# Optimization experiments

Hardware: AMD Instinct MI355X
Metric: run time of the kernel (lower is better)

## Reference

```python
import jax, jax.numpy as jnp
import numpy as np

NUM_CODONS = 64  # len(CODON_MAP_DNA)


def setup_inputs() -> dict:
    key = jax.random.key(0)
    k1, k2, k3, k4 = jax.random.split(key, 4)
    B, S = 16384, 2048
    rna_data = jax.random.randint(k1, (B, S), 0, 65, dtype=jnp.int64 if jax.config.read('jax_enable_x64') else jnp.int32)
    tissue_id = jax.random.randint(k2, (B,), 0, 30, dtype=jnp.int32)
    W = jax.random.normal(k3, (1, NUM_CODONS), dtype=jnp.float32)
    b = jax.random.normal(k4, (1,), dtype=jnp.float32)
    return {"rna_data": rna_data, "tissue_id": tissue_id, "W": W, "b": b}


def _frequencies(rna_data):
    # Batched histogram: counts[b, v] = #{s : rna_data[b, s] == v}, v in [0, 65)
    B = rna_data.shape[0]
    counts = jnp.zeros((B, NUM_CODONS + 1), dtype=jnp.float32)
    counts = counts.at[jnp.arange(B)[:, None], rna_data].add(1.0)
    counts = counts[:, 1:NUM_CODONS + 1]  # drop padding bin 0 -> [B, 64]
    return counts / jnp.sum(counts, axis=1, keepdims=True)


def reference(rna_data, tissue_id, W, b):
    freqs = _frequencies(rna_data)          # [B, 64]
    y_pred = freqs @ W.T + b                # [B, 1]
    return y_pred
```

## Files before the change

kernel.cpp:

```cpp
#include <hip/hip_runtime.h>


__global__ __launch_bounds__(256) void codon_freq_dot_kernel(
    const int* __restrict__ rna,
    const float* __restrict__ W,
    const float* __restrict__ b,
    float* __restrict__ out,
    int S)
{
    __shared__ float Wl[64];
    __shared__ float psum[4];
    __shared__ int   pcnt[4];

    const int row = blockIdx.x;
    const int t   = threadIdx.x;

    if (t < 64) Wl[t] = W[t];
    __syncthreads();

    const int4* p = reinterpret_cast<const int4*>(rna + (size_t)row * (size_t)S);
    const int nvec = S >> 2;

    float sum = 0.0f;
    int   cnt = 0;

    for (int i = t; i < nvec; i += 256) {
        int4 v = p[i];
        int e;
        e = v.x; if (e > 0) { sum += Wl[e - 1]; ++cnt; }
        e = v.y; if (e > 0) { sum += Wl[e - 1]; ++cnt; }
        e = v.z; if (e > 0) { sum += Wl[e - 1]; ++cnt; }
        e = v.w; if (e > 0) { sum += Wl[e - 1]; ++cnt; }
    }

    #pragma unroll
    for (int off = 32; off > 0; off >>= 1) {
        sum += __shfl_down(sum, off, 64);
        cnt += __shfl_down(cnt, off, 64);
    }

    const int wave = t >> 6;
    const int lane = t & 63;
    if (lane == 0) { psum[wave] = sum; pcnt[wave] = cnt; }
    __syncthreads();

    if (t == 0) {
        float s = psum[0] + psum[1] + psum[2] + psum[3];
        int   c = pcnt[0] + pcnt[1] + pcnt[2] + pcnt[3];
        out[row] = s / (float)c + b[0];
    }
}

extern "C" void kernel_launch(void* const* d_in, const int* in_sizes, int n_in,
                              void* d_out, int out_size, void* d_ws, size_t ws_size,
                              hipStream_t stream) {
    const int*   rna = (const int*)d_in[0];
    const float* W   = (const float*)d_in[2];
    const float* b   = (const float*)d_in[3];
    float*       out = (float*)d_out;

    const int B = out_size;
    const int S = in_sizes[0] / B;

    codon_freq_dot_kernel<<<B, 256, 0, stream>>>(rna, W, b, out, S);
}
```

Before: 25.97 us.

## Map one wavefront per row with fully unrolled nontemporal vector loads

Adds a specialized kernel for S=2048 where each wavefront handles a whole row, so a 256-thread block covers four rows. Each lane issues eight 16-byte nontemporal loads up front, and the row is reduced with wave shuffles only, with no shared-memory partials or second barrier. This is meant to raise memory-level parallelism, cut per-row block overhead and avoid polluting the cache on a streaming read. The generic kernel gains a scalar fallback for S not divisible by 4, and the fast path applies only when S is 2048 and B is a multiple of 4.

```diff
diff --git a/kernel.cpp b/kernel.cpp
--- a/kernel.cpp
+++ b/kernel.cpp
@@ -1,5 +1,52 @@
 #include <hip/hip_runtime.h>
 
+
+typedef int int4v __attribute__((ext_vector_type(4)));
+
+template<int NV>
+__global__ __launch_bounds__(256) void codon_rows_kernel(
+    const int* __restrict__ rna,
+    const float* __restrict__ W,
+    const float* __restrict__ b,
+    float* __restrict__ out,
+    int S)
+{
+    __shared__ float Wl[64];
+    const int t = threadIdx.x;
+    if (t < 64) Wl[t] = W[t];
+    __syncthreads();
+
+    const int wave = t >> 6;
+    const int lane = t & 63;
+    const int row  = blockIdx.x * 4 + wave;
+
+    const int4v* p = reinterpret_cast<const int4v*>(rna + (size_t)row * (size_t)S);
+
+    int4v v[NV];
+    #pragma unroll
+    for (int k = 0; k < NV; ++k)
+        v[k] = __builtin_nontemporal_load(&p[lane + 64 * k]);
+
+    float sum = 0.0f;
+    int   cnt = 0;
+    #pragma unroll
+    for (int k = 0; k < NV; ++k) {
+        #pragma unroll
+        for (int j = 0; j < 4; ++j) {
+            int e = v[k][j];
+            if (e > 0) { sum += Wl[e - 1]; ++cnt; }
+        }
+    }
+
+    #pragma unroll
+    for (int off = 32; off > 0; off >>= 1) {
+        sum += __shfl_down(sum, off, 64);
+        cnt += __shfl_down(cnt, off, 64);
+    }
+
+    if (lane == 0)
+        out[row] = sum / (float)cnt + b[0];
+}
 
 __global__ __launch_bounds__(256) void codon_freq_dot_kernel(
     const int* __restrict__ rna,
@@ -18,19 +65,27 @@
     if (t < 64) Wl[t] = W[t];
     __syncthreads();
 
-    const int4* p = reinterpret_cast<const int4*>(rna + (size_t)row * (size_t)S);
-    const int nvec = S >> 2;
+    const int* base = rna + (size_t)row * (size_t)S;
 
     float sum = 0.0f;
     int   cnt = 0;
 
-    for (int i = t; i < nvec; i += 256) {
-        int4 v = p[i];
-        int e;
-        e = v.x; if (e > 0) { sum += Wl[e - 1]; ++cnt; }
-        e = v.y; if (e > 0) { sum += Wl[e - 1]; ++cnt; }
-        e = v.z; if (e > 0) { sum += Wl[e - 1]; ++cnt; }
-        e = v.w; if (e > 0) { sum += Wl[e - 1]; ++cnt; }
+    if ((S & 3) == 0) {
+        const int4* p = reinterpret_cast<const int4*>(base);
+        const int nvec = S >> 2;
+        for (int i = t; i < nvec; i += 256) {
+            int4 v = p[i];
+            int e;
+            e = v.x; if (e > 0) { sum += Wl[e - 1]; ++cnt; }
+            e = v.y; if (e > 0) { sum += Wl[e - 1]; ++cnt; }
+            e = v.z; if (e > 0) { sum += Wl[e - 1]; ++cnt; }
+            e = v.w; if (e > 0) { sum += Wl[e - 1]; ++cnt; }
+        }
+    } else {
+        for (int i = t; i < S; i += 256) {
+            int e = base[i];
+            if (e > 0) { sum += Wl[e - 1]; ++cnt; }
+        }
     }
 
     #pragma unroll
@@ -62,5 +117,9 @@
     const int B = out_size;
     const int S = in_sizes[0] / B;
 
-    codon_freq_dot_kernel<<<B, 256, 0, stream>>>(rna, W, b, out, S);
+    if (S == 2048 && (B & 3) == 0) {
+        codon_rows_kernel<8><<<B / 4, 256, 0, stream>>>(rna, W, b, out, S);
+    } else {
+        codon_freq_dot_kernel<<<B, 256, 0, stream>>>(rna, W, b, out, S);
+    }
 }
```

Result: faster. 24.30 us (-6.4%).
